# Optimization experiments

Measured on AMD Instinct MI355X. Metric: run time of the kernel, lower is better.

## Reference

```python
import jax, jax.numpy as jnp
import numpy as np

W_BITS = 8
A_BITS = 8


def sym_quant(x, num_bits):
    # Symmetric per-last-dim abs-max quantization (SymQuantizer.forward, ndim<=3,
    # layerwise=False): s = (2^(b-1)-1)/(max|x| + 1e-6); q = round(x*s)/(s+1e-6)
    max_abs = jnp.max(jnp.abs(x), axis=-1, keepdims=True)
    s = (2.0 ** (num_bits - 1) - 1.0) / (max_abs + 1e-6)
    return jnp.round(x * s) / (s + 1e-6)


def setup_inputs() -> dict:
    key = jax.random.key(0)
    kx, kw = jax.random.split(key)
    B, S, NX, NF = 4, 2048, 1600, 6400
    x = jax.random.normal(kx, (B, S, NX), dtype=jnp.float32)
    weight = 0.02 * jax.random.normal(kw, (NX, NF), dtype=jnp.float32)  # Conv1D: [nx, nf]
    bias = jnp.zeros((NF,), dtype=jnp.float32)
    return {"x": x, "weight": weight, "bias": bias}


def reference(x, weight, bias):
    # quantize weights per-row (over nf), quantize activations per-token (over nx)
    wq = sym_quant(weight, W_BITS)
    xq = sym_quant(x, A_BITS)
    # addmm(bias, x.view(-1, nx), weight) then reshape back
    return jnp.einsum("bsx,xf->bsf", xq, wq) + bias
```

## Files before the change

### kernel.cpp

```cpp
#include <hip/hip_runtime.h>
#include <stdint.h>

typedef _Float16 f16;
typedef _Float16 f16x4 __attribute__((ext_vector_type(4)));
typedef _Float16 f16x8 __attribute__((ext_vector_type(8)));
typedef float f32x4 __attribute__((ext_vector_type(4)));

#define K_DIM 1600
#define NF_DIM 6400
#define KPAD 1664
#define NKT 26

__device__ __forceinline__ void async_copy16(const void* g, void* l) {
    __builtin_amdgcn_global_load_lds(
        (const __attribute__((address_space(1))) void*)(uintptr_t)g,
        (__attribute__((address_space(3))) void*)(uint32_t)(uintptr_t)l,
        16, 0, 0);
}

__device__ __forceinline__ float blockMax(float v, float* sm) {
#pragma unroll
    for (int off = 32; off > 0; off >>= 1)
        v = fmaxf(v, __shfl_down(v, off, 64));
    int wid = threadIdx.x >> 6, lane = threadIdx.x & 63;
    if (lane == 0) sm[wid] = v;
    __syncthreads();
    if (threadIdx.x == 0) {
        float m = sm[0];
        for (int i = 1; i < (int)(blockDim.x >> 6); ++i) m = fmaxf(m, sm[i]);
        sm[0] = m;
    }
    __syncthreads();
    return sm[0];
}

__global__ void quant_x_kernel(const float* __restrict__ x, f16* __restrict__ qx,
                               float* __restrict__ ax) {
    __shared__ float sm[4];
    size_t row = blockIdx.x;
    const float* xr = x + row * (size_t)K_DIM;
    float m = 0.f;
    const int n4 = K_DIM >> 2;
    for (int i = threadIdx.x; i < n4; i += blockDim.x) {
        float4 v = ((const float4*)xr)[i];
        m = fmaxf(fmaxf(fmaxf(fabsf(v.x), fabsf(v.y)), fmaxf(fabsf(v.z), fabsf(v.w))), m);
    }
    m = blockMax(m, sm);
    float s = 127.0f / (m + 1e-6f);
    if (threadIdx.x == 0) ax[row] = 1.0f / (s + 1e-6f);
    f16* qr = qx + row * (size_t)KPAD;
    for (int i = threadIdx.x; i < n4; i += blockDim.x) {
        float4 v = ((const float4*)xr)[i];
        f16x4 q;
        q[0] = (f16)rintf(v.x * s);
        q[1] = (f16)rintf(v.y * s);
        q[2] = (f16)rintf(v.z * s);
        q[3] = (f16)rintf(v.w * s);
        *(f16x4*)&qr[i * 4] = q;
    }
    if (threadIdx.x < 16) {
        f16x4 z = {};
        *(f16x4*)&qr[K_DIM + threadIdx.x * 4] = z;
    }
}

__global__ void wscale_kernel(const float* __restrict__ w, float* __restrict__ sw) {
    __shared__ float sm[4];
    size_t k = blockIdx.x;
    const float* wr = w + k * (size_t)NF_DIM;
    float m = 0.f;
    const int n4 = NF_DIM >> 2;
    for (int i = threadIdx.x; i < n4; i += blockDim.x) {
        float4 v = ((const float4*)wr)[i];
        m = fmaxf(fmaxf(fmaxf(fabsf(v.x), fabsf(v.y)), fmaxf(fabsf(v.z), fabsf(v.w))), m);
    }
    m = blockMax(m, sm);
    if (threadIdx.x == 0) sw[k] = 127.0f / (m + 1e-6f);
}

__global__ void wtq_kernel(const float* __restrict__ w, const float* __restrict__ sw,
                           f16* __restrict__ wqt) {
    __shared__ f16 t[64][80];
    int k0 = blockIdx.x * 64;
    int f0 = blockIdx.y * 64;
    int tid = threadIdx.x;
    if (k0 >= K_DIM) {
        int fr = tid >> 2;
        int ch = (tid & 3) << 4;
        float4 z = {};
        float4* dst = (float4*)&wqt[(size_t)(f0 + fr) * KPAD + k0 + ch];
        dst[0] = z;
        dst[1] = z;
        return;
    }
    int rr = tid >> 4;
    int cc = (tid & 15) << 2;
#pragma unroll
    for (int i = 0; i < 4; ++i) {
        int r = rr + i * 16;
        float s = sw[k0 + r];
        float inv = 1.0f / (s + 1e-6f);
        float4 v = *(const float4*)&w[(size_t)(k0 + r) * NF_DIM + f0 + cc];
        t[cc + 0][r] = (f16)(rintf(v.x * s) * inv);
        t[cc + 1][r] = (f16)(rintf(v.y * s) * inv);
        t[cc + 2][r] = (f16)(rintf(v.z * s) * inv);
        t[cc + 3][r] = (f16)(rintf(v.w * s) * inv);
    }
    __syncthreads();
    int fr = tid >> 2;
    int ch = (tid & 3) << 4;
    const float4* src = (const float4*)&t[fr][ch];
    float4* dst = (float4*)&wqt[(size_t)(f0 + fr) * KPAD + k0 + ch];
    dst[0] = src[0];
    dst[1] = src[1];
}

__global__ __launch_bounds__(512, 1) void gemm256(
    const f16* __restrict__ A,
    const f16* __restrict__ Bt,
    const float* __restrict__ ax,
    const float* __restrict__ bias,
    float* __restrict__ C, int M, int N) {
    extern __shared__ char lds[];

    const int tid = threadIdx.x;
    const int lane = tid & 63;
    const int wv = tid >> 6;
    const int wm = wv >> 2;
    const int wn = wv & 3;
    const int lr = lane & 15;
    const int lg = lane >> 4;

    const int nTn = N / 256;
    const int bid = blockIdx.x;
    const int cpx = gridDim.x >> 3;
    const int swz = (bid & 7) * cpx + (bid >> 3);
    const int tm = swz / nTn, tn = swz % nTn;
    const size_t m0 = (size_t)tm * 256, n0 = (size_t)tn * 256;

    const int srow8 = lane >> 3;
    const int sslot = (lane & 7) ^ srow8;

#define STAGE_HALF(mat, grow0, kbyte, ldst)                                          \
    {                                                                                \
        _Pragma("unroll") for (int j_ = 0; j_ < 2; ++j_) {                           \
            int L_ = (wv * 2 + j_) * 1024 + lane * 16;                               \
            int row_ = wv * 16 + j_ * 8 + srow8;                                     \
            const char* g_ = (const char*)((mat) + ((grow0) + row_) * (size_t)KPAD)  \
                             + (kbyte) + sslot * 16;                                 \
            async_copy16(g_, (ldst) + L_);                                           \
        }                                                                            \
    }
#define ST_ALO(buf, t) STAGE_HALF(A,  m0,       (t) * 128, (buf))
#define ST_AHI(buf, t) STAGE_HALF(A,  m0 + 128, (t) * 128, (buf) + 16384)
#define ST_BLO(buf, t) STAGE_HALF(Bt, n0,       (t) * 128, (buf) + 32768)
#define ST_BHI(buf, t) STAGE_HALF(Bt, n0 + 128, (t) * 128, (buf) + 49152)

#define LDF(base, row, s) \
    (*(const f16x8*)((base) + (row) * 128 + ((((s) ^ ((row) & 7))) << 4)))

#define RD_ALO(Ab)                                                           \
    { _Pragma("unroll") for (int mi_ = 0; mi_ < 4; ++mi_)                    \
      _Pragma("unroll") for (int kk_ = 0; kk_ < 2; ++kk_)                    \
          alo[mi_][kk_] = LDF((Ab), wm * 128 + mi_ * 16 + lr, kk_ * 4 + lg); }
#define RD_AHI(Ab)                                                           \
    { _Pragma("unroll") for (int mi_ = 0; mi_ < 4; ++mi_)                    \
      _Pragma("unroll") for (int kk_ = 0; kk_ < 2; ++kk_)                    \
          ahi[mi_][kk_] = LDF((Ab), wm * 128 + 64 + mi_ * 16 + lr, kk_ * 4 + lg); }
#define RD_BLO(Bb)                                                           \
    { _Pragma("unroll") for (int ni_ = 0; ni_ < 2; ++ni_)                    \
      _Pragma("unroll") for (int kk_ = 0; kk_ < 2; ++kk_)                    \
          blo[ni_][kk_] = LDF((Bb), wn * 64 + ni_ * 16 + lr, kk_ * 4 + lg); }
#define RD_BHI(Bb)                                                           \
    { _Pragma("unroll") for (int ni_ = 0; ni_ < 2; ++ni_)                    \
      _Pragma("unroll") for (int kk_ = 0; kk_ < 2; ++kk_)                    \
          bhi[ni_][kk_] = LDF((Bb), wn * 64 + 32 + ni_ * 16 + lr, kk_ * 4 + lg); }

#define BARRIER __builtin_amdgcn_s_barrier()
#define LGKM0 asm volatile("s_waitcnt lgkmcnt(0)" ::: "memory")
#define SB0 __builtin_amdgcn_sched_barrier(0)
#define VM4 asm volatile("s_waitcnt vmcnt(4)" ::: "memory")

#define MF(AF, BF, R0, C0)                                                        \
    {                                                                             \
        __builtin_amdgcn_s_setprio(1);                                            \
        _Pragma("unroll") for (int mi_ = 0; mi_ < 4; ++mi_)                       \
        _Pragma("unroll") for (int ni_ = 0; ni_ < 2; ++ni_)                       \
        _Pragma("unroll") for (int kk_ = 0; kk_ < 2; ++kk_)                       \
            acc[(R0) + mi_][(C0) + ni_] = __builtin_amdgcn_mfma_f32_16x16x32_f16( \
                AF[mi_][kk_], BF[ni_][kk_], acc[(R0) + mi_][(C0) + ni_], 0, 0, 0);\
        __builtin_amdgcn_s_setprio(0);                                            \
    }

    f32x4 acc[8][4] = {};
    char* buf0 = lds;
    char* buf1 = lds + 65536;
    const char* Ab0 = buf0;
    const char* Bb0 = buf0 + 32768;
    const char* Ab1 = buf1;
    const char* Bb1 = buf1 + 32768;

    ST_ALO(buf0, 0);
    ST_AHI(buf0, 0);
    ST_BLO(buf0, 0);
    ST_BHI(buf0, 0);
    ST_BLO(buf1, 1);
    ST_BHI(buf1, 1);
    VM4;
    BARRIER;

    for (int i = 0; i < NKT / 2; ++i) {
        const int t1s = 2 * i + 1;
        const int tp2 = (2 * i + 2 < NKT) ? 2 * i + 2 : NKT - 1;
        const int tp3 = (2 * i + 3 < NKT) ? 2 * i + 3 : NKT - 1;
        f16x8 alo[4][2], ahi[4][2], blo[2][2], bhi[2][2];

        RD_ALO(Ab0);
        RD_BLO(Bb0);
        ST_ALO(buf1, t1s);
        BARRIER; LGKM0; SB0;
        MF(alo, blo, 0, 0);
        BARRIER;

        RD_BHI(Bb0);
        ST_AHI(buf1, t1s);
        BARRIER; LGKM0; SB0;
        MF(alo, bhi, 0, 2);
        BARRIER;

        RD_AHI(Ab0);
        ST_BLO(buf0, tp2);
        BARRIER; LGKM0; SB0;
        MF(ahi, blo, 4, 0);
        BARRIER;

        ST_BHI(buf0, tp2);
        VM4;
        BARRIER; SB0;
        MF(ahi, bhi, 4, 2);
        BARRIER;

        RD_ALO(Ab1);
        RD_BLO(Bb1);
        ST_ALO(buf0, tp2);
        BARRIER; LGKM0; SB0;
        MF(alo, blo, 0, 0);
        BARRIER;

        RD_BHI(Bb1);
        ST_AHI(buf0, tp2);
        BARRIER; LGKM0; SB0;
        MF(alo, bhi, 0, 2);
        BARRIER;

        RD_AHI(Ab1);
        ST_BLO(buf1, tp3);
        BARRIER; LGKM0; SB0;
        MF(ahi, blo, 4, 0);
        BARRIER;

        ST_BHI(buf1, tp3);
        VM4;
        BARRIER; SB0;
        MF(ahi, bhi, 4, 2);
        BARRIER;
    }
    asm volatile("s_waitcnt vmcnt(0)" ::: "memory");

#pragma unroll
    for (int mi = 0; mi < 8; ++mi) {
#pragma unroll
        for (int j = 0; j < 4; ++j) {
            size_t mg = m0 + wm * 128 + mi * 16 + lg * 4 + j;
            float axv = ax[mg];
            float* crow = C + mg * (size_t)N + n0 + wn * 64;
#pragma unroll
            for (int ni = 0; ni < 4; ++ni) {
                int ng = ni * 16 + lr;
                crow[ng] = acc[mi][ni][j] * axv + bias[n0 + wn * 64 + ng];
            }
        }
    }
}

extern "C" void kernel_launch(void* const* d_in, const int* in_sizes, int n_in,
                              void* d_out, int out_size, void* d_ws, size_t ws_size,
                              hipStream_t stream) {
    const float* x = (const float*)d_in[0];
    const float* w = (const float*)d_in[1];
    const float* bias = (const float*)d_in[2];
    float* out = (float*)d_out;

    const int M = in_sizes[0] / K_DIM;
    const int N = NF_DIM;

    char* ws = (char*)d_ws;
    f16* qx = (f16*)ws;
    f16* wqt = (f16*)(ws + (size_t)M * KPAD * 2);
    float* ax = (float*)(ws + (size_t)M * KPAD * 2 + (size_t)N * KPAD * 2);
    float* sw = ax + M;

    quant_x_kernel<<<M, 256, 0, stream>>>(x, qx, ax);
    wscale_kernel<<<K_DIM, 256, 0, stream>>>(w, sw);
    wtq_kernel<<<dim3(KPAD / 64, NF_DIM / 64), 256, 0, stream>>>(w, sw, wqt);

    (void)hipFuncSetAttribute((const void*)gemm256,
                              hipFuncAttributeMaxDynamicSharedMemorySize, 131072);
    gemm256<<<(M / 256) * (N / 256), 512, 131072, stream>>>(qx, wqt, ax, bias, out, M, N);
}
```

Before: 262.8 us.

## Stage GEMM epilogue through LDS for coalesced float4 stores; precompute staging pointers

The output epilogue now writes each 16-row accumulator slab into padded LDS and then reads it back so every wave stores full 256-float rows with float4 writes. This replaces the scattered 4-byte stores of the old epilogue and should make better use of memory bandwidth for the large fp32 output. The global-to-LDS staging and LDS fragment reads now use precomputed base pointers and swizzle offsets instead of macros that recomputed addresses each time. The trade-off is extra barriers and LDS traffic in the epilogue.

```diff
diff --git a/kernel.cpp b/kernel.cpp
--- a/kernel.cpp
+++ b/kernel.cpp
@@ -10,6 +10,7 @@
 #define NF_DIM 6400
 #define KPAD 1664
 #define NKT 26
+#define KPB (KPAD * 2)
 
 __device__ __forceinline__ void async_copy16(const void* g, void* l) {
     __builtin_amdgcn_global_load_lds(
@@ -140,41 +141,60 @@
 
     const int srow8 = lane >> 3;
     const int sslot = (lane & 7) ^ srow8;
-
-#define STAGE_HALF(mat, grow0, kbyte, ldst)                                          \
-    {                                                                                \
-        _Pragma("unroll") for (int j_ = 0; j_ < 2; ++j_) {                           \
-            int L_ = (wv * 2 + j_) * 1024 + lane * 16;                               \
-            int row_ = wv * 16 + j_ * 8 + srow8;                                     \
-            const char* g_ = (const char*)((mat) + ((grow0) + row_) * (size_t)KPAD)  \
-                             + (kbyte) + sslot * 16;                                 \
-            async_copy16(g_, (ldst) + L_);                                           \
-        }                                                                            \
-    }
-#define ST_ALO(buf, t) STAGE_HALF(A,  m0,       (t) * 128, (buf))
-#define ST_AHI(buf, t) STAGE_HALF(A,  m0 + 128, (t) * 128, (buf) + 16384)
-#define ST_BLO(buf, t) STAGE_HALF(Bt, n0,       (t) * 128, (buf) + 32768)
-#define ST_BHI(buf, t) STAGE_HALF(Bt, n0 + 128, (t) * 128, (buf) + 49152)
-
-#define LDF(base, row, s) \
-    (*(const f16x8*)((base) + (row) * 128 + ((((s) ^ ((row) & 7))) << 4)))
-
-#define RD_ALO(Ab)                                                           \
-    { _Pragma("unroll") for (int mi_ = 0; mi_ < 4; ++mi_)                    \
-      _Pragma("unroll") for (int kk_ = 0; kk_ < 2; ++kk_)                    \
-          alo[mi_][kk_] = LDF((Ab), wm * 128 + mi_ * 16 + lr, kk_ * 4 + lg); }
-#define RD_AHI(Ab)                                                           \
-    { _Pragma("unroll") for (int mi_ = 0; mi_ < 4; ++mi_)                    \
-      _Pragma("unroll") for (int kk_ = 0; kk_ < 2; ++kk_)                    \
-          ahi[mi_][kk_] = LDF((Ab), wm * 128 + 64 + mi_ * 16 + lr, kk_ * 4 + lg); }
-#define RD_BLO(Bb)                                                           \
-    { _Pragma("unroll") for (int ni_ = 0; ni_ < 2; ++ni_)                    \
-      _Pragma("unroll") for (int kk_ = 0; kk_ < 2; ++kk_)                    \
-          blo[ni_][kk_] = LDF((Bb), wn * 64 + ni_ * 16 + lr, kk_ * 4 + lg); }
-#define RD_BHI(Bb)                                                           \
-    { _Pragma("unroll") for (int ni_ = 0; ni_ < 2; ++ni_)                    \
-      _Pragma("unroll") for (int kk_ = 0; kk_ < 2; ++kk_)                    \
-          bhi[ni_][kk_] = LDF((Bb), wn * 64 + 32 + ni_ * 16 + lr, kk_ * 4 + lg); }
+    const char* pAlo = (const char*)A + (m0 + (size_t)(wv * 16 + srow8)) * KPB + sslot * 16;
+    const char* pAhi = pAlo + (size_t)128 * KPB;
+    const char* pBlo = (const char*)Bt + (n0 + (size_t)(wv * 16 + srow8)) * KPB + sslot * 16;
+    const char* pBhi = pBlo + (size_t)128 * KPB;
+    const int L0 = wv * 2048 + lane * 16;
+
+#define ST(gp, t, roff)                                       \
+    {                                                         \
+        const char* g_ = (gp) + (size_t)(t) * 128;            \
+        async_copy16(g_, lds + (roff) + L0);                  \
+        async_copy16(g_ + 8 * KPB, lds + (roff) + L0 + 1024); \
+    }
+
+    const int swz0 = ((lg) ^ (lr & 7)) << 4;
+    const int swz1 = ((4 + lg) ^ (lr & 7)) << 4;
+    const int rbA = (wm * 128 + lr) * 128;
+    const int rbB = 32768 + (wn * 64 + lr) * 128;
+
+#define RD_ALO(bsel)                                                 \
+    {                                                                \
+        const char* p0_ = lds + (bsel) + rbA + swz0;                 \
+        const char* p1_ = lds + (bsel) + rbA + swz1;                 \
+        _Pragma("unroll") for (int mi_ = 0; mi_ < 4; ++mi_) {        \
+            alo[mi_][0] = *(const f16x8*)(p0_ + mi_ * 2048);         \
+            alo[mi_][1] = *(const f16x8*)(p1_ + mi_ * 2048);         \
+        }                                                            \
+    }
+#define RD_AHI(bsel)                                                 \
+    {                                                                \
+        const char* p0_ = lds + (bsel) + rbA + swz0 + 8192;          \
+        const char* p1_ = lds + (bsel) + rbA + swz1 + 8192;          \
+        _Pragma("unroll") for (int mi_ = 0; mi_ < 4; ++mi_) {        \
+            ahi[mi_][0] = *(const f16x8*)(p0_ + mi_ * 2048);         \
+            ahi[mi_][1] = *(const f16x8*)(p1_ + mi_ * 2048);         \
+        }                                                            \
+    }
+#define RD_BLO(bsel)                                                 \
+    {                                                                \
+        const char* p0_ = lds + (bsel) + rbB + swz0;                 \
+        const char* p1_ = lds + (bsel) + rbB + swz1;                 \
+        _Pragma("unroll") for (int ni_ = 0; ni_ < 2; ++ni_) {        \
+            blo[ni_][0] = *(const f16x8*)(p0_ + ni_ * 2048);         \
+            blo[ni_][1] = *(const f16x8*)(p1_ + ni_ * 2048);         \
+        }                                                            \
+    }
+#define RD_BHI(bsel)                                                 \
+    {                                                                \
+        const char* p0_ = lds + (bsel) + rbB + swz0 + 4096;          \
+        const char* p1_ = lds + (bsel) + rbB + swz1 + 4096;          \
+        _Pragma("unroll") for (int ni_ = 0; ni_ < 2; ++ni_) {        \
+            bhi[ni_][0] = *(const f16x8*)(p0_ + ni_ * 2048);         \
+            bhi[ni_][1] = *(const f16x8*)(p1_ + ni_ * 2048);         \
+        }                                                            \
+    }
 
 #define BARRIER __builtin_amdgcn_s_barrier()
 #define LGKM0 asm volatile("s_waitcnt lgkmcnt(0)" ::: "memory")
@@ -193,19 +213,14 @@
     }
 
     f32x4 acc[8][4] = {};
-    char* buf0 = lds;
-    char* buf1 = lds + 65536;
-    const char* Ab0 = buf0;
-    const char* Bb0 = buf0 + 32768;
-    const char* Ab1 = buf1;
-    const char* Bb1 = buf1 + 32768;
-
-    ST_ALO(buf0, 0);
-    ST_AHI(buf0, 0);
-    ST_BLO(buf0, 0);
-    ST_BHI(buf0, 0);
-    ST_BLO(buf1, 1);
-    ST_BHI(buf1, 1);
+    const int b0 = 0, b1 = 65536;
+
+    ST(pAlo, 0, b0 + 0);
+    ST(pAhi, 0, b0 + 16384);
+    ST(pBlo, 0, b0 + 32768);
+    ST(pBhi, 0, b0 + 49152);
+    ST(pBlo, 1, b1 + 32768);
+    ST(pBhi, 1, b1 + 49152);
     VM4;
     BARRIER;
 
@@ -215,70 +230,86 @@
         const int tp3 = (2 * i + 3 < NKT) ? 2 * i + 3 : NKT - 1;
         f16x8 alo[4][2], ahi[4][2], blo[2][2], bhi[2][2];
 
-        RD_ALO(Ab0);
-        RD_BLO(Bb0);
-        ST_ALO(buf1, t1s);
+        RD_ALO(b0);
+        RD_BLO(b0);
+        ST(pAlo, t1s, b1 + 0);
         BARRIER; LGKM0; SB0;
         MF(alo, blo, 0, 0);
         BARRIER;
 
-        RD_BHI(Bb0);
-        ST_AHI(buf1, t1s);
+        RD_BHI(b0);
+        ST(pAhi, t1s, b1 + 16384);
         BARRIER; LGKM0; SB0;
         MF(alo, bhi, 0, 2);
         BARRIER;
 
-        RD_AHI(Ab0);
-        ST_BLO(buf0, tp2);
+        RD_AHI(b0);
+        ST(pBlo, tp2, b0 + 32768);
         BARRIER; LGKM0; SB0;
         MF(ahi, blo, 4, 0);
         BARRIER;
 
-        ST_BHI(buf0, tp2);
+        ST(pBhi, tp2, b0 + 49152);
         VM4;
         BARRIER; SB0;
         MF(ahi, bhi, 4, 2);
         BARRIER;
 
-        RD_ALO(Ab1);
-        RD_BLO(Bb1);
-        ST_ALO(buf0, tp2);
+        RD_ALO(b1);
+        RD_BLO(b1);
+        ST(pAlo, tp2, b0 + 0);
         BARRIER; LGKM0; SB0;
         MF(alo, blo, 0, 0);
         BARRIER;
 
-        RD_BHI(Bb1);
-        ST_AHI(buf0, tp2);
+        RD_BHI(b1);
+        ST(pAhi, tp2, b0 + 16384);
         BARRIER; LGKM0; SB0;
         MF(alo, bhi, 0, 2);
         BARRIER;
 
-        RD_AHI(Ab1);
-        ST_BLO(buf1, tp3);
+        RD_AHI(b1);
+        ST(pBlo, tp3, b1 + 32768);
         BARRIER; LGKM0; SB0;
         MF(ahi, blo, 4, 0);
         BARRIER;
 
-        ST_BHI(buf1, tp3);
+        ST(pBhi, tp3, b1 + 49152);
         VM4;
         BARRIER; SB0;
         MF(ahi, bhi, 4, 2);
         BARRIER;
     }
     asm volatile("s_waitcnt vmcnt(0)" ::: "memory");
-
+    __syncthreads();
+
+    const float4 b4 = *(const float4*)&bias[n0 + lane * 4];
+    float* wbase = (float*)lds + wv * 1088;
 #pragma unroll
     for (int mi = 0; mi < 8; ++mi) {
-#pragma unroll
-        for (int j = 0; j < 4; ++j) {
-            size_t mg = m0 + wm * 128 + mi * 16 + lg * 4 + j;
+        __syncthreads();
+#pragma unroll
+        for (int ni = 0; ni < 4; ++ni)
+#pragma unroll
+            for (int j = 0; j < 4; ++j)
+                wbase[(lg * 4 + j) * 68 + ni * 16 + lr] = acc[mi][ni][j];
+        __syncthreads();
+#pragma unroll
+        for (int k = 0; k < 4; ++k) {
+            int rr = wv * 4 + k;
+            int wmp = rr >> 4, r16 = rr & 15;
+            size_t mg = m0 + wmp * 128 + (mi & 3) * 16 + ((mi >> 2) * 0) + mi * 0 +
+                        ((mi < 4) ? mi * 16 : (mi - 4) * 16) * 0;
+            mg = m0 + wmp * 128 + mi * 16 + r16;
             float axv = ax[mg];
-            float* crow = C + mg * (size_t)N + n0 + wn * 64;
-#pragma unroll
-            for (int ni = 0; ni < 4; ++ni) {
-                int ng = ni * 16 + lr;
-                crow[ng] = acc[mi][ni][j] * axv + bias[n0 + wn * 64 + ng];
-            }
+            int wvp = wmp * 4 + (lane >> 4);
+            float4 v = *(const float4*)((const float*)lds + wvp * 1088 + r16 * 68 + (lane & 15) * 4);
+            float4 o;
+            o.x = v.x * axv + b4.x;
+            o.y = v.y * axv + b4.y;
+            o.z = v.z * axv + b4.z;
+            o.w = v.w * axv + b4.w;
+            *(float4*)&C[mg * (size_t)N + n0 + lane * 4] = o;
         }
     }
 }
```

Measured after the change: 240.5 us. 8.5% less time.

## Retile GEMM to 128x320 blocks with register double-buffered fragments

Applied to the files above, without the earlier changes.

Replaces the 256x256 output tile with a 128x320 tile so the grid (64x20 = 1280 blocks) divides more evenly across the CUs, and restructures the main loop so each k-tile is split into four MFMA phases. A/B fragments are double-buffered in registers with partial lgkmcnt waits, and there is one barrier per k-tile instead of several. Global-to-LDS staging is simplified with precomputed base pointers and a smaller LDS footprint. Arithmetic intensity per block drops, which raises global and L2 traffic per FLOP, and the finer-grained waits add risk to scheduling correctness.

```diff
diff --git a/kernel.cpp b/kernel.cpp
--- a/kernel.cpp
+++ b/kernel.cpp
@@ -10,6 +10,10 @@
 #define NF_DIM 6400
 #define KPAD 1664
 #define NKT 26
+#define KPB (KPAD * 2)
+
+#define BUFSZ 57344
+#define BOFF 16384
 
 __device__ __forceinline__ void async_copy16(const void* g, void* l) {
     __builtin_amdgcn_global_load_lds(
@@ -115,7 +119,7 @@
     dst[1] = src[1];
 }
 
-__global__ __launch_bounds__(512, 1) void gemm256(
+__global__ __launch_bounds__(512, 1) void gemm128x320(
     const f16* __restrict__ A,
     const f16* __restrict__ Bt,
     const float* __restrict__ ax,
@@ -131,154 +135,124 @@
     const int lr = lane & 15;
     const int lg = lane >> 4;
 
-    const int nTn = N / 256;
     const int bid = blockIdx.x;
     const int cpx = gridDim.x >> 3;
     const int swz = (bid & 7) * cpx + (bid >> 3);
-    const int tm = swz / nTn, tn = swz % nTn;
-    const size_t m0 = (size_t)tm * 256, n0 = (size_t)tn * 256;
+    const int tm = swz & 63;
+    const int tn = swz >> 6;
+    const size_t m0 = (size_t)tm * 128, n0 = (size_t)tn * 320;
 
     const int srow8 = lane >> 3;
     const int sslot = (lane & 7) ^ srow8;
-
-#define STAGE_HALF(mat, grow0, kbyte, ldst)                                          \
-    {                                                                                \
-        _Pragma("unroll") for (int j_ = 0; j_ < 2; ++j_) {                           \
-            int L_ = (wv * 2 + j_) * 1024 + lane * 16;                               \
-            int row_ = wv * 16 + j_ * 8 + srow8;                                     \
-            const char* g_ = (const char*)((mat) + ((grow0) + row_) * (size_t)KPAD)  \
-                             + (kbyte) + sslot * 16;                                 \
-            async_copy16(g_, (ldst) + L_);                                           \
-        }                                                                            \
-    }
-#define ST_ALO(buf, t) STAGE_HALF(A,  m0,       (t) * 128, (buf))
-#define ST_AHI(buf, t) STAGE_HALF(A,  m0 + 128, (t) * 128, (buf) + 16384)
-#define ST_BLO(buf, t) STAGE_HALF(Bt, n0,       (t) * 128, (buf) + 32768)
-#define ST_BHI(buf, t) STAGE_HALF(Bt, n0 + 128, (t) * 128, (buf) + 49152)
-
-#define LDF(base, row, s) \
-    (*(const f16x8*)((base) + (row) * 128 + ((((s) ^ ((row) & 7))) << 4)))
-
-#define RD_ALO(Ab)                                                           \
-    { _Pragma("unroll") for (int mi_ = 0; mi_ < 4; ++mi_)                    \
-      _Pragma("unroll") for (int kk_ = 0; kk_ < 2; ++kk_)                    \
-          alo[mi_][kk_] = LDF((Ab), wm * 128 + mi_ * 16 + lr, kk_ * 4 + lg); }
-#define RD_AHI(Ab)                                                           \
-    { _Pragma("unroll") for (int mi_ = 0; mi_ < 4; ++mi_)                    \
-      _Pragma("unroll") for (int kk_ = 0; kk_ < 2; ++kk_)                    \
-          ahi[mi_][kk_] = LDF((Ab), wm * 128 + 64 + mi_ * 16 + lr, kk_ * 4 + lg); }
-#define RD_BLO(Bb)                                                           \
-    { _Pragma("unroll") for (int ni_ = 0; ni_ < 2; ++ni_)                    \
-      _Pragma("unroll") for (int kk_ = 0; kk_ < 2; ++kk_)                    \
-          blo[ni_][kk_] = LDF((Bb), wn * 64 + ni_ * 16 + lr, kk_ * 4 + lg); }
-#define RD_BHI(Bb)                                                           \
-    { _Pragma("unroll") for (int ni_ = 0; ni_ < 2; ++ni_)                    \
-      _Pragma("unroll") for (int kk_ = 0; kk_ < 2; ++kk_)                    \
-          bhi[ni_][kk_] = LDF((Bb), wn * 64 + 32 + ni_ * 16 + lr, kk_ * 4 + lg); }
+    const char* pA = (const char*)A + (m0 + (size_t)(wv * 8 + srow8)) * KPB + sslot * 16;
+    const char* pB = (const char*)Bt + (n0 + (size_t)(wv * 8 + srow8)) * KPB + sslot * 16;
+    const int L0 = wv * 1024 + lane * 16;
+
+#define ST_A(bufo, t)                                                          \
+    {                                                                          \
+        const char* g_ = pA + (size_t)(t) * 128;                               \
+        async_copy16(g_, lds + (bufo) + L0);                                   \
+        async_copy16(g_ + (size_t)64 * KPB, lds + (bufo) + 8192 + L0);         \
+    }
+#define ST_B(bufo, t)                                                          \
+    {                                                                          \
+        const char* g_ = pB + (size_t)(t) * 128;                               \
+        _Pragma("unroll") for (int c_ = 0; c_ < 5; ++c_)                       \
+            async_copy16(g_ + (size_t)(c_ * 64) * KPB,                         \
+                         lds + (bufo) + BOFF + c_ * 8192 + L0);                \
+    }
+
+    const int swz0 = ((lg) ^ (lr & 7)) << 4;
+    const int swz1 = ((4 + lg) ^ (lr & 7)) << 4;
+    const int rbA = (wm * 64 + lr) * 128;
+    const int rbB = BOFF + wn * 10240 + lr * 128;
+
+#define RD_A(dst, bufo, rowoff, sz)                                    \
+    {                                                                  \
+        const char* p_ = lds + (bufo) + rbA + (rowoff) + (sz);         \
+        dst[0] = *(const f16x8*)(p_);                                  \
+        dst[1] = *(const f16x8*)(p_ + 2048);                           \
+    }
+#define RD_B(dst, bufo, sz)                                            \
+    {                                                                  \
+        const char* p_ = lds + (bufo) + rbB + (sz);                    \
+        _Pragma("unroll") for (int n_ = 0; n_ < 5; ++n_)               \
+            dst[n_] = *(const f16x8*)(p_ + n_ * 2048);                 \
+    }
 
 #define BARRIER __builtin_amdgcn_s_barrier()
-#define LGKM0 asm volatile("s_waitcnt lgkmcnt(0)" ::: "memory")
+#define LGKM(n) asm volatile("s_waitcnt lgkmcnt(" #n ")" ::: "memory")
+#define VM0 asm volatile("s_waitcnt vmcnt(0)" ::: "memory")
 #define SB0 __builtin_amdgcn_sched_barrier(0)
-#define VM4 asm volatile("s_waitcnt vmcnt(4)" ::: "memory")
-
-#define MF(AF, BF, R0, C0)                                                        \
+
+#define MF25(AF, BF, R0)                                                          \
     {                                                                             \
         __builtin_amdgcn_s_setprio(1);                                            \
-        _Pragma("unroll") for (int mi_ = 0; mi_ < 4; ++mi_)                       \
-        _Pragma("unroll") for (int ni_ = 0; ni_ < 2; ++ni_)                       \
-        _Pragma("unroll") for (int kk_ = 0; kk_ < 2; ++kk_)                       \
-            acc[(R0) + mi_][(C0) + ni_] = __builtin_amdgcn_mfma_f32_16x16x32_f16( \
-                AF[mi_][kk_], BF[ni_][kk_], acc[(R0) + mi_][(C0) + ni_], 0, 0, 0);\
+        _Pragma("unroll") for (int a_ = 0; a_ < 2; ++a_)                          \
+        _Pragma("unroll") for (int n_ = 0; n_ < 5; ++n_)                          \
+            acc[(R0) + a_][n_] = __builtin_amdgcn_mfma_f32_16x16x32_f16(          \
+                AF[a_], BF[n_], acc[(R0) + a_][n_], 0, 0, 0);                     \
         __builtin_amdgcn_s_setprio(0);                                            \
     }
 
-    f32x4 acc[8][4] = {};
-    char* buf0 = lds;
-    char* buf1 = lds + 65536;
-    const char* Ab0 = buf0;
-    const char* Bb0 = buf0 + 32768;
-    const char* Ab1 = buf1;
-    const char* Bb1 = buf1 + 32768;
-
-    ST_ALO(buf0, 0);
-    ST_AHI(buf0, 0);
-    ST_BLO(buf0, 0);
-    ST_BHI(buf0, 0);
-    ST_BLO(buf1, 1);
-    ST_BHI(buf1, 1);
-    VM4;
+#define TILE(CUR, NXT, tcur, tnext)                                   \
+    {                                                                 \
+                     \
+        RD_A(aN, CUR, 0, swz1);                                       \
+        RD_B(B1, CUR, swz1);                                          \
+        ST_A(NXT, tnext);                                             \
+        LGKM(7); SB0;                               \
+        MF25(aP, B0, 0);                                              \
+                             \
+        RD_A(aP, CUR, 4096, swz0);                                    \
+        ST_B(NXT, tnext);                                             \
+        LGKM(2); SB0;                               \
+        MF25(aN, B1, 0);                                              \
+                                           \
+        RD_A(aN, CUR, 4096, swz1);                                    \
+        LGKM(2); SB0;                         \
+        MF25(aP, B0, 2);                                              \
+            \
+        VM0;                                                          \
+        BARRIER; SB0;                           \
+        RD_A(aP, NXT, 0, swz0);                                       \
+        RD_B(B0, NXT, swz0);                                          \
+        LGKM(7); SB0;                         \
+        MF25(aN, B1, 2);                                              \
+        BARRIER;                       \
+    }
+
+    f32x4 acc[4][5] = {};
+    f16x8 aP[2], aN[2], B0[5], B1[5];
+
+    ST_A(0, 0);
+    ST_B(0, 0);
+    VM0;
     BARRIER;
+    RD_A(aP, 0, 0, swz0);
+    RD_B(B0, 0, swz0);
 
     for (int i = 0; i < NKT / 2; ++i) {
-        const int t1s = 2 * i + 1;
-        const int tp2 = (2 * i + 2 < NKT) ? 2 * i + 2 : NKT - 1;
-        const int tp3 = (2 * i + 3 < NKT) ? 2 * i + 3 : NKT - 1;
-        f16x8 alo[4][2], ahi[4][2], blo[2][2], bhi[2][2];
-
-        RD_ALO(Ab0);
-        RD_BLO(Bb0);
-        ST_ALO(buf1, t1s);
-        BARRIER; LGKM0; SB0;
-        MF(alo, blo, 0, 0);
-        BARRIER;
-
-        RD_BHI(Bb0);
-        ST_AHI(buf1, t1s);
-        BARRIER; LGKM0; SB0;
-        MF(alo, bhi, 0, 2);
-        BARRIER;
-
-        RD_AHI(Ab0);
-        ST_BLO(buf0, tp2);
-        BARRIER; LGKM0; SB0;
-        MF(ahi, blo, 4, 0);
-        BARRIER;
-
-        ST_BHI(buf0, tp2);
-        VM4;
-        BARRIER; SB0;
-        MF(ahi, bhi, 4, 2);
-        BARRIER;
-
-        RD_ALO(Ab1);
-        RD_BLO(Bb1);
-        ST_ALO(buf0, tp2);
-        BARRIER; LGKM0; SB0;
-        MF(alo, blo, 0, 0);
-        BARRIER;
-
-        RD_BHI(Bb1);
-        ST_AHI(buf0, tp2);
-        BARRIER; LGKM0; SB0;
-        MF(alo, bhi, 0, 2);
-        BARRIER;
-
-        RD_AHI(Ab1);
-        ST_BLO(buf1, tp3);
-        BARRIER; LGKM0; SB0;
-        MF(ahi, blo, 4, 0);
-        BARRIER;
-
-        ST_BHI(buf1, tp3);
-        VM4;
-        BARRIER; SB0;
-        MF(ahi, bhi, 4, 2);
-        BARRIER;
-    }
-    asm volatile("s_waitcnt vmcnt(0)" ::: "memory");
-
-#pragma unroll
-    for (int mi = 0; mi < 8; ++mi) {
+        const int te = 2 * i + 1;
+        const int to = (2 * i + 2 < NKT) ? 2 * i + 2 : NKT - 1;
+        TILE(0, BUFSZ, 2 * i, te);
+        TILE(BUFSZ, 0, 2 * i + 1, to);
+    }
+    asm volatile("s_waitcnt vmcnt(0) lgkmcnt(0)" ::: "memory");
+
+    float bv[5];
+#pragma unroll
+    for (int n_ = 0; n_ < 5; ++n_) bv[n_] = bias[n0 + wn * 80 + n_ * 16 + lr];
+#pragma unroll
+    for (int a = 0; a < 4; ++a) {
 #pragma unroll
         for (int j = 0; j < 4; ++j) {
-            size_t mg = m0 + wm * 128 + mi * 16 + lg * 4 + j;
-            float axv = ax[mg];
-            float* crow = C + mg * (size_t)N + n0 + wn * 64;
-#pragma unroll
-            for (int ni = 0; ni < 4; ++ni) {
-                int ng = ni * 16 + lr;
-                crow[ng] = acc[mi][ni][j] * axv + bias[n0 + wn * 64 + ng];
-            }
+            size_t row = m0 + wm * 64 + a * 16 + lg * 4 + j;
+            float axv = ax[row];
+            float* crow = C + row * (size_t)N + n0 + wn * 80;
+#pragma unroll
+            for (int n_ = 0; n_ < 5; ++n_)
+                crow[n_ * 16 + lr] = acc[a][n_][j] * axv + bv[n_];
         }
     }
 }
@@ -304,7 +278,7 @@
     wscale_kernel<<<K_DIM, 256, 0, stream>>>(w, sw);
     wtq_kernel<<<dim3(KPAD / 64, NF_DIM / 64), 256, 0, stream>>>(w, sw, wqt);
 
-    (void)hipFuncSetAttribute((const void*)gemm256,
-                              hipFuncAttributeMaxDynamicSharedMemorySize, 131072);
-    gemm256<<<(M / 256) * (N / 256), 512, 131072, stream>>>(qx, wqt, ax, bias, out, M, N);
-}
+    (void)hipFuncSetAttribute((const void*)gemm128x320,
+                              hipFuncAttributeMaxDynamicSharedMemorySize, 2 * BUFSZ);
+    gemm128x320<<<(M / 128) * (N / 320), 512, 2 * BUFSZ, stream>>>(qx, wqt, ax, bias, out, M, N);
+}
```

New measurement: 254.9 us. 1.03x faster.
